# Kernel optimization log

Measured on AMD Instinct MI355X. Metric: run time of the kernel, lower is better.

## Reference

```python
import jax, jax.numpy as jnp
import numpy as np

# 8 voxel corner offsets in {0,1}^3 (order matches signed offsets in the
# torch module after the *0.5+0.5 remap used inside splitting/trilinear calls)
_CORNERS = np.array([[1,1,1],[1,1,0],[1,0,1],[0,1,1],[1,0,0],[0,1,0],[0,0,1],[0,0,0]], dtype=np.float32)

K = 150000   # unique corner keys (embedding rows)
V = 100000   # voxels
N = 262144   # query samples (rays * steps)
D = 64       # quantized_embed_dim


def setup_inputs() -> dict:
    key = jax.random.key(0)
    k1, k2, k3, k4, k5 = jax.random.split(key, 5)
    values = jax.random.normal(k1, (K, D), dtype=jnp.float32)
    p = jax.random.uniform(k2, (N, 3), dtype=jnp.float32)            # local trilinear coords in [0,1]
    W_proj = jax.random.normal(k3, (D, D), dtype=jnp.float32) / np.sqrt(D)
    b_proj = jnp.zeros((D,), dtype=jnp.float32)
    feats = jax.random.randint(k4, (V, 8), 0, K, dtype=jnp.int64) if jax.config.read('jax_enable_x64') else jax.random.randint(k4, (V, 8), 0, K).astype(jnp.int32)
    sample_vidx = jax.random.randint(k5, (N,), 0, V).astype(jnp.int32)
    return {"values": values, "p": p, "W_proj": W_proj, "b_proj": b_proj,
            "feats": feats, "sample_vidx": sample_vidx}


def trilinear_interp(p, q, corner_feats):
    # p: [N,3] in [0,1]; q: [8,3] corners in {0,1}; corner_feats: [N,8,D]
    # weight per corner = prod_d (p*q + (1-p)*(1-q))  -- identical to NSVF trilinear_interp
    w = jnp.prod(p[:, None, :] * q[None] + (1.0 - p[:, None, :]) * (1.0 - q[None]), axis=-1)  # [N,8]
    return jnp.einsum('nc,ncd->nd', w, corner_feats)


def reference(values, p, W_proj, b_proj, feats, sample_vidx):
    q = jnp.asarray(_CORNERS)
    corner_idx = feats[sample_vidx]          # [N,8] irregular gather of corner keys
    corner_feats = values[corner_idx]        # [N,8,D] embedding gather
    feat = trilinear_interp(p, q, corner_feats)   # [N,D]
    out = feat @ W_proj + b_proj             # values_proj Linear(embed_dim, embed_dim)
    return out
```

## Files before the change

### kernel.cpp

```cpp
#include <hip/hip_runtime.h>

#define TPB 256

typedef __attribute__((ext_vector_type(8))) short bf16x8;
typedef __attribute__((ext_vector_type(4))) float f32x4;

__device__ __forceinline__ unsigned pack_bf16_rne(float lo, float hi) {
    union { float f; unsigned u; } a, b;
    a.f = lo; b.f = hi;
    unsigned ua = (a.u + 0x7fffu + ((a.u >> 16) & 1u)) >> 16;
    unsigned ub = (b.u + 0x7fffu + ((b.u >> 16) & 1u)) >> 16;
    return ua | (ub << 16);
}
__device__ __forceinline__ float bf_lo(unsigned u) {
    union { unsigned i; float f; } c; c.i = u << 16; return c.f;
}
__device__ __forceinline__ float bf_hi(unsigned u) {
    union { unsigned i; float f; } c; c.i = u & 0xffff0000u; return c.f;
}

__global__ __launch_bounds__(TPB) void cvt_inputs(
    const float4* __restrict__ src, uint4* __restrict__ dst, int n8,
    const float* __restrict__ W, uint4* __restrict__ wfrag, int nvb)
{
    if ((int)blockIdx.x == nvb) {
        const int t = threadIdx.x;
        for (int e = t; e < 512; e += TPB) {
            const int l  = e & 63;
            const int f  = e >> 6;
            const int ct = f >> 1;
            const int kf = f & 1;
            const int col = ct * 16 + (l & 15);
            const int k0  = kf * 32 + 8 * (l >> 4);
            uint4 o;
            o.x = pack_bf16_rne(W[(k0 + 0) * 64 + col], W[(k0 + 1) * 64 + col]);
            o.y = pack_bf16_rne(W[(k0 + 2) * 64 + col], W[(k0 + 3) * 64 + col]);
            o.z = pack_bf16_rne(W[(k0 + 4) * 64 + col], W[(k0 + 5) * 64 + col]);
            o.w = pack_bf16_rne(W[(k0 + 6) * 64 + col], W[(k0 + 7) * 64 + col]);
            wfrag[e] = o;
        }
        return;
    }
    const int i = blockIdx.x * TPB + threadIdx.x;
    if (i < n8) {
        const float4 a = src[2 * i];
        const float4 b = src[2 * i + 1];
        uint4 o;
        o.x = pack_bf16_rne(a.x, a.y);
        o.y = pack_bf16_rne(a.z, a.w);
        o.z = pack_bf16_rne(b.x, b.y);
        o.w = pack_bf16_rne(b.z, b.w);
        dst[i] = o;
    }
}

__global__ __launch_bounds__(TPB, 2) void fused_embed_proj_mfma(
    const unsigned* __restrict__ valbf,
    const float* __restrict__ p,
    const uint4* __restrict__ wfrag,
    const float* __restrict__ b,
    const int*   __restrict__ feats,
    const int*   __restrict__ vidx,
    float* __restrict__ out,
    int N)
{
    const int t    = threadIdx.x;
    const int l    = t & 63;
    const int w    = t >> 6;
    const int base = blockIdx.x * 64 + 16 * w;
    const int srow = l & 15;
    const int kq   = l >> 4;

    int n = base + srow;
    if (n >= N) n = N - 1;

    const int v = vidx[n];
    const int4 f0 = *(const int4*)&feats[(size_t)v * 8];
    const int4 f1 = *(const int4*)&feats[(size_t)v * 8 + 4];

    const float px = p[n * 3 + 0];
    const float py = p[n * 3 + 1];
    const float pz = p[n * 3 + 2];
    const float ox = 1.0f - px, oy = 1.0f - py, oz = 1.0f - pz;
    float wgt[8];
    wgt[0] = px * py * pz;
    wgt[1] = px * py * oz;
    wgt[2] = px * oy * pz;
    wgt[3] = ox * py * pz;
    wgt[4] = px * oy * oz;
    wgt[5] = ox * py * oz;
    wgt[6] = ox * oy * pz;
    wgt[7] = ox * oy * oz;
    const int cidx[8] = {f0.x, f0.y, f0.z, f0.w, f1.x, f1.y, f1.z, f1.w};

    uint4 q0s[8], q1s[8];
    #pragma unroll
    for (int c = 0; c < 8; ++c) {
        const unsigned* row = valbf + (size_t)cidx[c] * 32;
        q0s[c] = *(const uint4*)(row + 4 * kq);
        q1s[c] = *(const uint4*)(row + 16 + 4 * kq);
    }

    float a0[8] = {0.f,0.f,0.f,0.f,0.f,0.f,0.f,0.f};
    float a1[8] = {0.f,0.f,0.f,0.f,0.f,0.f,0.f,0.f};
    #pragma unroll
    for (int c = 0; c < 8; ++c) {
        const uint4 q0 = q0s[c];
        const uint4 q1 = q1s[c];
        const float wc = wgt[c];
        a0[0] = fmaf(wc, bf_lo(q0.x), a0[0]);
        a0[1] = fmaf(wc, bf_hi(q0.x), a0[1]);
        a0[2] = fmaf(wc, bf_lo(q0.y), a0[2]);
        a0[3] = fmaf(wc, bf_hi(q0.y), a0[3]);
        a0[4] = fmaf(wc, bf_lo(q0.z), a0[4]);
        a0[5] = fmaf(wc, bf_hi(q0.z), a0[5]);
        a0[6] = fmaf(wc, bf_lo(q0.w), a0[6]);
        a0[7] = fmaf(wc, bf_hi(q0.w), a0[7]);
        a1[0] = fmaf(wc, bf_lo(q1.x), a1[0]);
        a1[1] = fmaf(wc, bf_hi(q1.x), a1[1]);
        a1[2] = fmaf(wc, bf_lo(q1.y), a1[2]);
        a1[3] = fmaf(wc, bf_hi(q1.y), a1[3]);
        a1[4] = fmaf(wc, bf_lo(q1.z), a1[4]);
        a1[5] = fmaf(wc, bf_hi(q1.z), a1[5]);
        a1[6] = fmaf(wc, bf_lo(q1.w), a1[6]);
        a1[7] = fmaf(wc, bf_hi(q1.w), a1[7]);
    }

    bf16x8 afrag0, afrag1;
    {
        union { unsigned u[4]; bf16x8 v; } cv;
        cv.u[0] = pack_bf16_rne(a0[0], a0[1]);
        cv.u[1] = pack_bf16_rne(a0[2], a0[3]);
        cv.u[2] = pack_bf16_rne(a0[4], a0[5]);
        cv.u[3] = pack_bf16_rne(a0[6], a0[7]);
        afrag0 = cv.v;
        cv.u[0] = pack_bf16_rne(a1[0], a1[1]);
        cv.u[1] = pack_bf16_rne(a1[2], a1[3]);
        cv.u[2] = pack_bf16_rne(a1[4], a1[5]);
        cv.u[3] = pack_bf16_rne(a1[6], a1[7]);
        afrag1 = cv.v;
    }

    #pragma unroll
    for (int ct = 0; ct < 4; ++ct) {
        const float bias = b[ct * 16 + srow];
        f32x4 acc;
        acc[0] = bias; acc[1] = bias; acc[2] = bias; acc[3] = bias;
        union { uint4 u; bf16x8 v; } b0, b1;
        b0.u = wfrag[(ct * 2 + 0) * 64 + l];
        b1.u = wfrag[(ct * 2 + 1) * 64 + l];
        acc = __builtin_amdgcn_mfma_f32_16x16x32_bf16(afrag0, b0.v, acc, 0, 0, 0);
        acc = __builtin_amdgcn_mfma_f32_16x16x32_bf16(afrag1, b1.v, acc, 0, 0, 0);

        const int col = ct * 16 + srow;
        #pragma unroll
        for (int r = 0; r < 4; ++r) {
            const int n2 = base + 4 * kq + r;
            if (n2 < N)
                __builtin_nontemporal_store(acc[r], &out[(size_t)n2 * 64 + col]);
        }
    }
}

__global__ __launch_bounds__(TPB) void fused_embed_proj_fp32(
    const float* __restrict__ values, const float* __restrict__ p,
    const float* __restrict__ W, const float* __restrict__ b,
    const int* __restrict__ feats, const int* __restrict__ vidx,
    float* __restrict__ out, int N)
{
    __shared__ float featS[64][68];
    __shared__ float Wlds[64][64];

    const int t    = threadIdx.x;
    const int base = blockIdx.x * 64;
    {
        const float4* Wv = (const float4*)W;
        float4*       Wl = (float4*)&Wlds[0][0];
        #pragma unroll
        for (int i = 0; i < 4; ++i) Wl[t + i * TPB] = Wv[t + i * TPB];
    }
    const int g  = t & 15;
    const int sb = t >> 4;

    int   cidx[4][8];
    float wgt[4][8];
    #pragma unroll
    for (int i = 0; i < 4; ++i) {
        const int s = sb + 16 * i;
        int n = base + s;
        if (n >= N) n = N - 1;
        const int v = vidx[n];
        const int4 f0 = *(const int4*)&feats[(size_t)v * 8];
        const int4 f1 = *(const int4*)&feats[(size_t)v * 8 + 4];
        cidx[i][0] = f0.x; cidx[i][1] = f0.y; cidx[i][2] = f0.z; cidx[i][3] = f0.w;
        cidx[i][4] = f1.x; cidx[i][5] = f1.y; cidx[i][6] = f1.z; cidx[i][7] = f1.w;
        const float px = p[n * 3], py = p[n * 3 + 1], pz = p[n * 3 + 2];
        const float ox = 1.f - px, oy = 1.f - py, oz = 1.f - pz;
        wgt[i][0] = px * py * pz; wgt[i][1] = px * py * oz;
        wgt[i][2] = px * oy * pz; wgt[i][3] = ox * py * pz;
        wgt[i][4] = px * oy * oz; wgt[i][5] = ox * py * oz;
        wgt[i][6] = ox * oy * pz; wgt[i][7] = ox * oy * oz;
    }
    #pragma unroll
    for (int i = 0; i < 4; ++i) {
        float4 acc; acc.x = acc.y = acc.z = acc.w = 0.f;
        #pragma unroll
        for (int c = 0; c < 8; ++c) {
            const float4 val = *(const float4*)&values[(size_t)cidx[i][c] * 64 + 4 * g];
            const float w = wgt[i][c];
            acc.x = fmaf(w, val.x, acc.x); acc.y = fmaf(w, val.y, acc.y);
            acc.z = fmaf(w, val.z, acc.z); acc.w = fmaf(w, val.w, acc.w);
        }
        *(float4*)&featS[sb + 16 * i][4 * g] = acc;
    }
    __syncthreads();

    const int tx = t & 15, ty = t >> 4;
    float acc[4][4];
    {
        const float4 bb = ((const float4*)b)[tx];
        #pragma unroll
        for (int j = 0; j < 4; ++j) {
            acc[j][0] = bb.x; acc[j][1] = bb.y; acc[j][2] = bb.z; acc[j][3] = bb.w;
        }
    }
    #pragma unroll 4
    for (int d = 0; d < 64; ++d) {
        const float a0 = featS[4 * ty + 0][d];
        const float a1 = featS[4 * ty + 1][d];
        const float a2 = featS[4 * ty + 2][d];
        const float a3 = featS[4 * ty + 3][d];
        const float4 wr = *(const float4*)&Wlds[d][4 * tx];
        acc[0][0] = fmaf(a0, wr.x, acc[0][0]); acc[0][1] = fmaf(a0, wr.y, acc[0][1]);
        acc[0][2] = fmaf(a0, wr.z, acc[0][2]); acc[0][3] = fmaf(a0, wr.w, acc[0][3]);
        acc[1][0] = fmaf(a1, wr.x, acc[1][0]); acc[1][1] = fmaf(a1, wr.y, acc[1][1]);
        acc[1][2] = fmaf(a1, wr.z, acc[1][2]); acc[1][3] = fmaf(a1, wr.w, acc[1][3]);
        acc[2][0] = fmaf(a2, wr.x, acc[2][0]); acc[2][1] = fmaf(a2, wr.y, acc[2][1]);
        acc[2][2] = fmaf(a2, wr.z, acc[2][2]); acc[2][3] = fmaf(a2, wr.w, acc[2][3]);
        acc[3][0] = fmaf(a3, wr.x, acc[3][0]); acc[3][1] = fmaf(a3, wr.y, acc[3][1]);
        acc[3][2] = fmaf(a3, wr.z, acc[3][2]); acc[3][3] = fmaf(a3, wr.w, acc[3][3]);
    }
    #pragma unroll
    for (int j = 0; j < 4; ++j) {
        const int n = base + 4 * ty + j;
        if (n < N) {
            float4 o; o.x = acc[j][0]; o.y = acc[j][1]; o.z = acc[j][2]; o.w = acc[j][3];
            *(float4*)&out[(size_t)n * 64 + 4 * tx] = o;
        }
    }
}

extern "C" void kernel_launch(void* const* d_in, const int* in_sizes, int n_in,
                              void* d_out, int out_size, void* d_ws, size_t ws_size,
                              hipStream_t stream) {
    const float* values = (const float*)d_in[0];
    const float* p      = (const float*)d_in[1];
    const float* W      = (const float*)d_in[2];
    const float* b      = (const float*)d_in[3];
    const int*   feats  = (const int*)d_in[4];
    const int*   vidx   = (const int*)d_in[5];
    float* out = (float*)d_out;

    const int N  = in_sizes[5];
    const int KD = in_sizes[0];
    const int nblocks = (N + 63) / 64;

    const size_t val_bytes = (size_t)KD * 2;
    const size_t need      = val_bytes + 8192;
    if (ws_size >= need) {
        unsigned* valbf = (unsigned*)d_ws;
        uint4*    wfrag = (uint4*)((char*)d_ws + val_bytes);
        const int n8  = KD / 8;
        const int nvb = (n8 + TPB - 1) / TPB;
        cvt_inputs<<<nvb + 1, TPB, 0, stream>>>(
            (const float4*)values, (uint4*)valbf, n8, W, wfrag, nvb);
        fused_embed_proj_mfma<<<nblocks, TPB, 0, stream>>>(
            valbf, p, wfrag, b, feats, vidx, out, N);
    } else {
        fused_embed_proj_fp32<<<nblocks, TPB, 0, stream>>>(
            values, p, W, b, feats, vidx, out, N);
    }
}
```

Measured before the change: 68.62 us.

## Project embedding table before gathering, replacing per-sample MFMA with table projection

Result: slower. 75.82 us (+10.5%).

```diff
diff --git a/kernel.cpp b/kernel.cpp
--- a/kernel.cpp
+++ b/kernel.cpp
@@ -19,45 +19,65 @@
     union { unsigned i; float f; } c; c.i = u & 0xffff0000u; return c.f;
 }
 
-__global__ __launch_bounds__(TPB) void cvt_inputs(
-    const float4* __restrict__ src, uint4* __restrict__ dst, int n8,
-    const float* __restrict__ W, uint4* __restrict__ wfrag, int nvb)
+__global__ __launch_bounds__(TPB) void proj_table_mfma(
+    const float* __restrict__ values,
+    const float* __restrict__ W,
+    unsigned short* __restrict__ vp,
+    int K)
 {
-    if ((int)blockIdx.x == nvb) {
-        const int t = threadIdx.x;
-        for (int e = t; e < 512; e += TPB) {
-            const int l  = e & 63;
-            const int f  = e >> 6;
-            const int ct = f >> 1;
-            const int kf = f & 1;
-            const int col = ct * 16 + (l & 15);
-            const int k0  = kf * 32 + 8 * (l >> 4);
-            uint4 o;
-            o.x = pack_bf16_rne(W[(k0 + 0) * 64 + col], W[(k0 + 1) * 64 + col]);
-            o.y = pack_bf16_rne(W[(k0 + 2) * 64 + col], W[(k0 + 3) * 64 + col]);
-            o.z = pack_bf16_rne(W[(k0 + 4) * 64 + col], W[(k0 + 5) * 64 + col]);
-            o.w = pack_bf16_rne(W[(k0 + 6) * 64 + col], W[(k0 + 7) * 64 + col]);
-            wfrag[e] = o;
-        }
-        return;
-    }
-    const int i = blockIdx.x * TPB + threadIdx.x;
-    if (i < n8) {
-        const float4 a = src[2 * i];
-        const float4 b = src[2 * i + 1];
-        uint4 o;
-        o.x = pack_bf16_rne(a.x, a.y);
-        o.y = pack_bf16_rne(a.z, a.w);
-        o.z = pack_bf16_rne(b.x, b.y);
-        o.w = pack_bf16_rne(b.z, b.w);
-        dst[i] = o;
-    }
-}
-
-__global__ __launch_bounds__(TPB, 2) void fused_embed_proj_mfma(
-    const unsigned* __restrict__ valbf,
+    const int t    = threadIdx.x;
+    const int l    = t & 63;
+    const int w    = t >> 6;
+    const int r0   = blockIdx.x * 64 + 16 * w;
+    const int srow = l & 15;
+    const int kq   = l >> 4;
+
+    int row = r0 + srow;
+    if (row >= K) row = K - 1;
+
+    bf16x8 af[2];
+    #pragma unroll
+    for (int kf = 0; kf < 2; ++kf) {
+        const float4 x0 = *(const float4*)&values[(size_t)row * 64 + kf * 32 + 8 * kq];
+        const float4 x1 = *(const float4*)&values[(size_t)row * 64 + kf * 32 + 8 * kq + 4];
+        union { unsigned u[4]; bf16x8 v; } cv;
+        cv.u[0] = pack_bf16_rne(x0.x, x0.y);
+        cv.u[1] = pack_bf16_rne(x0.z, x0.w);
+        cv.u[2] = pack_bf16_rne(x1.x, x1.y);
+        cv.u[3] = pack_bf16_rne(x1.z, x1.w);
+        af[kf] = cv.v;
+    }
+
+    #pragma unroll
+    for (int ct = 0; ct < 4; ++ct) {
+        const int col = ct * 16 + srow;
+        f32x4 acc;
+        acc[0] = 0.f; acc[1] = 0.f; acc[2] = 0.f; acc[3] = 0.f;
+        #pragma unroll
+        for (int kf = 0; kf < 2; ++kf) {
+            const int k0 = kf * 32 + 8 * kq;
+            union { unsigned u[4]; bf16x8 v; } bv;
+            bv.u[0] = pack_bf16_rne(W[(k0 + 0) * 64 + col], W[(k0 + 1) * 64 + col]);
+            bv.u[1] = pack_bf16_rne(W[(k0 + 2) * 64 + col], W[(k0 + 3) * 64 + col]);
+            bv.u[2] = pack_bf16_rne(W[(k0 + 4) * 64 + col], W[(k0 + 5) * 64 + col]);
+            bv.u[3] = pack_bf16_rne(W[(k0 + 6) * 64 + col], W[(k0 + 7) * 64 + col]);
+            acc = __builtin_amdgcn_mfma_f32_16x16x32_bf16(af[kf], bv.v, acc, 0, 0, 0);
+        }
+        #pragma unroll
+        for (int r = 0; r < 4; ++r) {
+            const int orow = r0 + 4 * kq + r;
+            if (orow < K) {
+                union { float f; unsigned u; } a; a.f = acc[r];
+                const unsigned us = (a.u + 0x7fffu + ((a.u >> 16) & 1u)) >> 16;
+                vp[(size_t)orow * 64 + col] = (unsigned short)us;
+            }
+        }
+    }
+}
+
+__global__ __launch_bounds__(TPB) void gather_interp(
+    const unsigned* __restrict__ vp,
     const float* __restrict__ p,
-    const uint4* __restrict__ wfrag,
     const float* __restrict__ b,
     const int*   __restrict__ feats,
     const int*   __restrict__ vidx,
@@ -71,8 +91,9 @@
     const int srow = l & 15;
     const int kq   = l >> 4;
 
+    const bool valid = (base + srow) < N;
     int n = base + srow;
-    if (n >= N) n = N - 1;
+    if (!valid) n = N - 1;
 
     const int v = vidx[n];
     const int4 f0 = *(const int4*)&feats[(size_t)v * 8];
@@ -96,7 +117,7 @@
     uint4 q0s[8], q1s[8];
     #pragma unroll
     for (int c = 0; c < 8; ++c) {
-        const unsigned* row = valbf + (size_t)cidx[c] * 32;
+        const unsigned* row = vp + (size_t)cidx[c] * 32;
         q0s[c] = *(const uint4*)(row + 4 * kq);
         q1s[c] = *(const uint4*)(row + 16 + 4 * kq);
     }
@@ -126,39 +147,28 @@
         a1[7] = fmaf(wc, bf_hi(q1.w), a1[7]);
     }
 
-    bf16x8 afrag0, afrag1;
-    {
-        union { unsigned u[4]; bf16x8 v; } cv;
-        cv.u[0] = pack_bf16_rne(a0[0], a0[1]);
-        cv.u[1] = pack_bf16_rne(a0[2], a0[3]);
-        cv.u[2] = pack_bf16_rne(a0[4], a0[5]);
-        cv.u[3] = pack_bf16_rne(a0[6], a0[7]);
-        afrag0 = cv.v;
-        cv.u[0] = pack_bf16_rne(a1[0], a1[1]);
-        cv.u[1] = pack_bf16_rne(a1[2], a1[3]);
-        cv.u[2] = pack_bf16_rne(a1[4], a1[5]);
-        cv.u[3] = pack_bf16_rne(a1[6], a1[7]);
-        afrag1 = cv.v;
-    }
-
-    #pragma unroll
-    for (int ct = 0; ct < 4; ++ct) {
-        const float bias = b[ct * 16 + srow];
-        f32x4 acc;
-        acc[0] = bias; acc[1] = bias; acc[2] = bias; acc[3] = bias;
-        union { uint4 u; bf16x8 v; } b0, b1;
-        b0.u = wfrag[(ct * 2 + 0) * 64 + l];
-        b1.u = wfrag[(ct * 2 + 1) * 64 + l];
-        acc = __builtin_amdgcn_mfma_f32_16x16x32_bf16(afrag0, b0.v, acc, 0, 0, 0);
-        acc = __builtin_amdgcn_mfma_f32_16x16x32_bf16(afrag1, b1.v, acc, 0, 0, 0);
-
-        const int col = ct * 16 + srow;
-        #pragma unroll
-        for (int r = 0; r < 4; ++r) {
-            const int n2 = base + 4 * kq + r;
-            if (n2 < N)
-                __builtin_nontemporal_store(acc[r], &out[(size_t)n2 * 64 + col]);
-        }
+    if (valid) {
+        const float4 b00 = *(const float4*)&b[8 * kq];
+        const float4 b01 = *(const float4*)&b[8 * kq + 4];
+        const float4 b10 = *(const float4*)&b[32 + 8 * kq];
+        const float4 b11 = *(const float4*)&b[32 + 8 * kq + 4];
+        float* o = out + (size_t)n * 64;
+        __builtin_nontemporal_store(a0[0] + b00.x, o + 8 * kq + 0);
+        __builtin_nontemporal_store(a0[1] + b00.y, o + 8 * kq + 1);
+        __builtin_nontemporal_store(a0[2] + b00.z, o + 8 * kq + 2);
+        __builtin_nontemporal_store(a0[3] + b00.w, o + 8 * kq + 3);
+        __builtin_nontemporal_store(a0[4] + b01.x, o + 8 * kq + 4);
+        __builtin_nontemporal_store(a0[5] + b01.y, o + 8 * kq + 5);
+        __builtin_nontemporal_store(a0[6] + b01.z, o + 8 * kq + 6);
+        __builtin_nontemporal_store(a0[7] + b01.w, o + 8 * kq + 7);
+        __builtin_nontemporal_store(a1[0] + b10.x, o + 32 + 8 * kq + 0);
+        __builtin_nontemporal_store(a1[1] + b10.y, o + 32 + 8 * kq + 1);
+        __builtin_nontemporal_store(a1[2] + b10.z, o + 32 + 8 * kq + 2);
+        __builtin_nontemporal_store(a1[3] + b10.w, o + 32 + 8 * kq + 3);
+        __builtin_nontemporal_store(a1[4] + b11.x, o + 32 + 8 * kq + 4);
+        __builtin_nontemporal_store(a1[5] + b11.y, o + 32 + 8 * kq + 5);
+        __builtin_nontemporal_store(a1[6] + b11.z, o + 32 + 8 * kq + 6);
+        __builtin_nontemporal_store(a1[7] + b11.w, o + 32 + 8 * kq + 7);
     }
 }
 
@@ -263,19 +273,16 @@
 
     const int N  = in_sizes[5];
     const int KD = in_sizes[0];
+    const int K  = KD / 64;
     const int nblocks = (N + 63) / 64;
 
-    const size_t val_bytes = (size_t)KD * 2;
-    const size_t need      = val_bytes + 8192;
+    const size_t need = (size_t)KD * 2;
     if (ws_size >= need) {
-        unsigned* valbf = (unsigned*)d_ws;
-        uint4*    wfrag = (uint4*)((char*)d_ws + val_bytes);
-        const int n8  = KD / 8;
-        const int nvb = (n8 + TPB - 1) / TPB;
-        cvt_inputs<<<nvb + 1, TPB, 0, stream>>>(
-            (const float4*)values, (uint4*)valbf, n8, W, wfrag, nvb);
-        fused_embed_proj_mfma<<<nblocks, TPB, 0, stream>>>(
-            valbf, p, wfrag, b, feats, vidx, out, N);
+        unsigned short* vp = (unsigned short*)d_ws;
+        const int kblocks = (K + 63) / 64;
+        proj_table_mfma<<<kblocks, TPB, 0, stream>>>(values, W, vp, K);
+        gather_interp<<<nblocks, TPB, 0, stream>>>(
+            (const unsigned*)vp, p, b, feats, vidx, out, N);
     } else {
         fused_embed_proj_fp32<<<nblocks, TPB, 0, stream>>>(
             values, p, W, b, feats, vidx, out, N);
```

## Counting-sort samples by voxel before gather to improve corner-row locality

Applied to the files above, without the earlier changes.

Result: slower. 81.66 us (+19.0%).

```diff
diff --git a/kernel.cpp b/kernel.cpp
--- a/kernel.cpp
+++ b/kernel.cpp
@@ -19,48 +19,130 @@
     union { unsigned i; float f; } c; c.i = u & 0xffff0000u; return c.f;
 }
 
-__global__ __launch_bounds__(TPB) void cvt_inputs(
-    const float4* __restrict__ src, uint4* __restrict__ dst, int n8,
-    const float* __restrict__ W, uint4* __restrict__ wfrag, int nvb)
-{
-    if ((int)blockIdx.x == nvb) {
-        const int t = threadIdx.x;
-        for (int e = t; e < 512; e += TPB) {
-            const int l  = e & 63;
-            const int f  = e >> 6;
-            const int ct = f >> 1;
-            const int kf = f & 1;
-            const int col = ct * 16 + (l & 15);
-            const int k0  = kf * 32 + 8 * (l >> 4);
+__global__ __launch_bounds__(TPB) void prep_combo(
+    const float4* __restrict__ src, uint4* __restrict__ dst, int n8, int nvb,
+    unsigned* __restrict__ cnt, int V, int zb,
+    const float* __restrict__ W, uint4* __restrict__ wfrag)
+{
+    int bid = blockIdx.x;
+    if (bid < nvb) {
+        const int i = bid * TPB + threadIdx.x;
+        if (i < n8) {
+            const float4 a = src[2 * i];
+            const float4 b = src[2 * i + 1];
             uint4 o;
-            o.x = pack_bf16_rne(W[(k0 + 0) * 64 + col], W[(k0 + 1) * 64 + col]);
-            o.y = pack_bf16_rne(W[(k0 + 2) * 64 + col], W[(k0 + 3) * 64 + col]);
-            o.z = pack_bf16_rne(W[(k0 + 4) * 64 + col], W[(k0 + 5) * 64 + col]);
-            o.w = pack_bf16_rne(W[(k0 + 6) * 64 + col], W[(k0 + 7) * 64 + col]);
-            wfrag[e] = o;
+            o.x = pack_bf16_rne(a.x, a.y);
+            o.y = pack_bf16_rne(a.z, a.w);
+            o.z = pack_bf16_rne(b.x, b.y);
+            o.w = pack_bf16_rne(b.z, b.w);
+            dst[i] = o;
         }
         return;
     }
+    bid -= nvb;
+    if (bid < zb) {
+        const int i = bid * TPB + threadIdx.x;
+        if (i < V) cnt[i] = 0u;
+        return;
+    }
+    const int t = threadIdx.x;
+    for (int e = t; e < 512; e += TPB) {
+        const int l  = e & 63;
+        const int f  = e >> 6;
+        const int ct = f >> 1;
+        const int kf = f & 1;
+        const int col = ct * 16 + (l & 15);
+        const int k0  = kf * 32 + 8 * (l >> 4);
+        uint4 o;
+        o.x = pack_bf16_rne(W[(k0 + 0) * 64 + col], W[(k0 + 1) * 64 + col]);
+        o.y = pack_bf16_rne(W[(k0 + 2) * 64 + col], W[(k0 + 3) * 64 + col]);
+        o.z = pack_bf16_rne(W[(k0 + 4) * 64 + col], W[(k0 + 5) * 64 + col]);
+        o.w = pack_bf16_rne(W[(k0 + 6) * 64 + col], W[(k0 + 7) * 64 + col]);
+        wfrag[e] = o;
+    }
+}
+
+__global__ __launch_bounds__(TPB) void hist_kernel(
+    const int* __restrict__ vidx, unsigned* __restrict__ cnt, int N) {
     const int i = blockIdx.x * TPB + threadIdx.x;
-    if (i < n8) {
-        const float4 a = src[2 * i];
-        const float4 b = src[2 * i + 1];
-        uint4 o;
-        o.x = pack_bf16_rne(a.x, a.y);
-        o.y = pack_bf16_rne(a.z, a.w);
-        o.z = pack_bf16_rne(b.x, b.y);
-        o.w = pack_bf16_rne(b.z, b.w);
-        dst[i] = o;
-    }
-}
-
-__global__ __launch_bounds__(TPB, 2) void fused_embed_proj_mfma(
+    if (i < N) atomicAdd(&cnt[vidx[i]], 1u);
+}
+
+__global__ __launch_bounds__(TPB) void scan1_kernel(
+    const unsigned* __restrict__ cnt, unsigned* __restrict__ loc,
+    unsigned* __restrict__ chunksum, int V)
+{
+    __shared__ unsigned part[TPB];
+    const int t    = threadIdx.x;
+    const int base = blockIdx.x * 2048 + t * 8;
+
+    unsigned e[8];
+    unsigned s = 0;
+    #pragma unroll
+    for (int j = 0; j < 8; ++j) {
+        e[j] = (base + j < V) ? cnt[base + j] : 0u;
+        s += e[j];
+    }
+    part[t] = s;
+    __syncthreads();
+    for (int d = 1; d < TPB; d <<= 1) {
+        unsigned v = (t >= d) ? part[t - d] : 0u;
+        __syncthreads();
+        part[t] += v;
+        __syncthreads();
+    }
+    unsigned run = part[t] - s;
+    #pragma unroll
+    for (int j = 0; j < 8; ++j) {
+        if (base + j < V) loc[base + j] = run;
+        run += e[j];
+    }
+    if (t == TPB - 1) chunksum[blockIdx.x] = part[TPB - 1];
+}
+
+__global__ __launch_bounds__(TPB) void scan2_kernel(
+    const unsigned* __restrict__ chunksum, unsigned* __restrict__ chunkpref, int nc)
+{
+    __shared__ unsigned part[TPB];
+    const int t = threadIdx.x;
+    unsigned s = (t < nc) ? chunksum[t] : 0u;
+    part[t] = s;
+    __syncthreads();
+    for (int d = 1; d < TPB; d <<= 1) {
+        unsigned v = (t >= d) ? part[t - d] : 0u;
+        __syncthreads();
+        part[t] += v;
+        __syncthreads();
+    }
+    if (t < nc) chunkpref[t] = part[t] - s;
+}
+
+__global__ __launch_bounds__(TPB) void scatter_kernel(
+    const int* __restrict__ vidx, const float* __restrict__ p,
+    unsigned* __restrict__ loc, const unsigned* __restrict__ chunkpref,
+    float4* __restrict__ psort, int* __restrict__ svox, int N)
+{
+    const int i = blockIdx.x * TPB + threadIdx.x;
+    if (i < N) {
+        const int v = vidx[i];
+        const unsigned pos = chunkpref[v >> 11] + atomicAdd(&loc[v], 1u);
+        float4 r;
+        r.x = p[3 * i + 0];
+        r.y = p[3 * i + 1];
+        r.z = p[3 * i + 2];
+        r.w = __int_as_float(i);
+        psort[pos] = r;
+        svox[pos]  = v;
+    }
+}
+
+__global__ __launch_bounds__(TPB) void gather_mfma_sorted(
     const unsigned* __restrict__ valbf,
-    const float* __restrict__ p,
+    const float4* __restrict__ psort,
+    const int*   __restrict__ svox,
     const uint4* __restrict__ wfrag,
     const float* __restrict__ b,
     const int*   __restrict__ feats,
-    const int*   __restrict__ vidx,
     float* __restrict__ out,
     int N)
 {
@@ -71,16 +153,16 @@
     const int srow = l & 15;
     const int kq   = l >> 4;
 
-    int n = base + srow;
-    if (n >= N) n = N - 1;
-
-    const int v = vidx[n];
+    const int slot = base + srow;
+    const int cs   = (slot < N) ? slot : N - 1;
+
+    const float4 rec = psort[cs];
+    const int v = svox[cs];
+
     const int4 f0 = *(const int4*)&feats[(size_t)v * 8];
     const int4 f1 = *(const int4*)&feats[(size_t)v * 8 + 4];
 
-    const float px = p[n * 3 + 0];
-    const float py = p[n * 3 + 1];
-    const float pz = p[n * 3 + 2];
+    const float px = rec.x, py = rec.y, pz = rec.z;
     const float ox = 1.0f - px, oy = 1.0f - py, oz = 1.0f - pz;
     float wgt[8];
     wgt[0] = px * py * pz;
@@ -141,6 +223,116 @@
         afrag1 = cv.v;
     }
 
+    int nrow[4];
+    #pragma unroll
+    for (int r = 0; r < 4; ++r) {
+        const int s2 = base + 4 * kq + r;
+        nrow[r] = (s2 < N) ? __float_as_int(psort[s2].w) : -1;
+    }
+
+    #pragma unroll
+    for (int ct = 0; ct < 4; ++ct) {
+        const float bias = b[ct * 16 + srow];
+        f32x4 acc;
+        acc[0] = bias; acc[1] = bias; acc[2] = bias; acc[3] = bias;
+        union { uint4 u; bf16x8 v; } b0, b1;
+        b0.u = wfrag[(ct * 2 + 0) * 64 + l];
+        b1.u = wfrag[(ct * 2 + 1) * 64 + l];
+        acc = __builtin_amdgcn_mfma_f32_16x16x32_bf16(afrag0, b0.v, acc, 0, 0, 0);
+        acc = __builtin_amdgcn_mfma_f32_16x16x32_bf16(afrag1, b1.v, acc, 0, 0, 0);
+
+        const int col = ct * 16 + srow;
+        #pragma unroll
+        for (int r = 0; r < 4; ++r) {
+            if (nrow[r] >= 0)
+                __builtin_nontemporal_store(acc[r], &out[(size_t)nrow[r] * 64 + col]);
+        }
+    }
+}
+
+__global__ __launch_bounds__(TPB) void fused_embed_proj_mfma(
+    const unsigned* __restrict__ valbf, const float* __restrict__ p,
+    const uint4* __restrict__ wfrag, const float* __restrict__ b,
+    const int* __restrict__ feats, const int* __restrict__ vidx,
+    float* __restrict__ out, int N)
+{
+    const int t    = threadIdx.x;
+    const int l    = t & 63;
+    const int w    = t >> 6;
+    const int base = blockIdx.x * 64 + 16 * w;
+    const int srow = l & 15;
+    const int kq   = l >> 4;
+
+    int n = base + srow;
+    if (n >= N) n = N - 1;
+
+    const int v = vidx[n];
+    const int4 f0 = *(const int4*)&feats[(size_t)v * 8];
+    const int4 f1 = *(const int4*)&feats[(size_t)v * 8 + 4];
+
+    const float px = p[n * 3 + 0];
+    const float py = p[n * 3 + 1];
+    const float pz = p[n * 3 + 2];
+    const float ox = 1.0f - px, oy = 1.0f - py, oz = 1.0f - pz;
+    float wgt[8];
+    wgt[0] = px * py * pz;
+    wgt[1] = px * py * oz;
+    wgt[2] = px * oy * pz;
+    wgt[3] = ox * py * pz;
+    wgt[4] = px * oy * oz;
+    wgt[5] = ox * py * oz;
+    wgt[6] = ox * oy * pz;
+    wgt[7] = ox * oy * oz;
+    const int cidx[8] = {f0.x, f0.y, f0.z, f0.w, f1.x, f1.y, f1.z, f1.w};
+
+    uint4 q0s[8], q1s[8];
+    #pragma unroll
+    for (int c = 0; c < 8; ++c) {
+        const unsigned* row = valbf + (size_t)cidx[c] * 32;
+        q0s[c] = *(const uint4*)(row + 4 * kq);
+        q1s[c] = *(const uint4*)(row + 16 + 4 * kq);
+    }
+
+    float a0[8] = {0.f,0.f,0.f,0.f,0.f,0.f,0.f,0.f};
+    float a1[8] = {0.f,0.f,0.f,0.f,0.f,0.f,0.f,0.f};
+    #pragma unroll
+    for (int c = 0; c < 8; ++c) {
+        const uint4 q0 = q0s[c];
+        const uint4 q1 = q1s[c];
+        const float wc = wgt[c];
+        a0[0] = fmaf(wc, bf_lo(q0.x), a0[0]);
+        a0[1] = fmaf(wc, bf_hi(q0.x), a0[1]);
+        a0[2] = fmaf(wc, bf_lo(q0.y), a0[2]);
+        a0[3] = fmaf(wc, bf_hi(q0.y), a0[3]);
+        a0[4] = fmaf(wc, bf_lo(q0.z), a0[4]);
+        a0[5] = fmaf(wc, bf_hi(q0.z), a0[5]);
+        a0[6] = fmaf(wc, bf_lo(q0.w), a0[6]);
+        a0[7] = fmaf(wc, bf_hi(q0.w), a0[7]);
+        a1[0] = fmaf(wc, bf_lo(q1.x), a1[0]);
+        a1[1] = fmaf(wc, bf_hi(q1.x), a1[1]);
+        a1[2] = fmaf(wc, bf_lo(q1.y), a1[2]);
+        a1[3] = fmaf(wc, bf_hi(q1.y), a1[3]);
+        a1[4] = fmaf(wc, bf_lo(q1.z), a1[4]);
+        a1[5] = fmaf(wc, bf_hi(q1.z), a1[5]);
+        a1[6] = fmaf(wc, bf_lo(q1.w), a1[6]);
+        a1[7] = fmaf(wc, bf_hi(q1.w), a1[7]);
+    }
+
+    bf16x8 afrag0, afrag1;
+    {
+        union { unsigned u[4]; bf16x8 v; } cv;
+        cv.u[0] = pack_bf16_rne(a0[0], a0[1]);
+        cv.u[1] = pack_bf16_rne(a0[2], a0[3]);
+        cv.u[2] = pack_bf16_rne(a0[4], a0[5]);
+        cv.u[3] = pack_bf16_rne(a0[6], a0[7]);
+        afrag0 = cv.v;
+        cv.u[0] = pack_bf16_rne(a1[0], a1[1]);
+        cv.u[1] = pack_bf16_rne(a1[2], a1[3]);
+        cv.u[2] = pack_bf16_rne(a1[4], a1[5]);
+        cv.u[3] = pack_bf16_rne(a1[6], a1[7]);
+        afrag1 = cv.v;
+    }
+
     #pragma unroll
     for (int ct = 0; ct < 4; ++ct) {
         const float bias = b[ct * 16 + srow];
@@ -263,17 +455,49 @@
 
     const int N  = in_sizes[5];
     const int KD = in_sizes[0];
+    const int V  = in_sizes[4] / 8;
     const int nblocks = (N + 63) / 64;
-
-    const size_t val_bytes = (size_t)KD * 2;
-    const size_t need      = val_bytes + 8192;
-    if (ws_size >= need) {
-        unsigned* valbf = (unsigned*)d_ws;
-        uint4*    wfrag = (uint4*)((char*)d_ws + val_bytes);
-        const int n8  = KD / 8;
-        const int nvb = (n8 + TPB - 1) / TPB;
-        cvt_inputs<<<nvb + 1, TPB, 0, stream>>>(
-            (const float4*)values, (uint4*)valbf, n8, W, wfrag, nvb);
+    const int n8  = KD / 8;
+    const int nvb = (n8 + TPB - 1) / TPB;
+    const int zb  = (V + TPB - 1) / TPB;
+    const int nchunks = (V + 2047) / 2048;
+
+    auto align256 = [](size_t x) { return (x + 255) & ~(size_t)255; };
+    const size_t valbf_off = 0;
+    const size_t wfrag_off = align256((size_t)KD * 2);
+    const size_t cnt_off   = wfrag_off + align256((size_t)8192);
+    const size_t loc_off   = cnt_off + align256((size_t)V * 4);
+    const size_t csum_off  = loc_off + align256((size_t)V * 4);
+    const size_t cpref_off = csum_off + align256((size_t)nchunks * 4);
+    const size_t psort_off = cpref_off + align256((size_t)nchunks * 4);
+    const size_t svox_off  = psort_off + align256((size_t)N * 16);
+    const size_t need_sort = svox_off + align256((size_t)N * 4);
+    const size_t need_mfma = wfrag_off + 8192;
+
+    if (ws_size >= need_sort && nchunks <= TPB) {
+        unsigned* valbf  = (unsigned*)((char*)d_ws + valbf_off);
+        uint4*    wfrag  = (uint4*)((char*)d_ws + wfrag_off);
+        unsigned* cnt    = (unsigned*)((char*)d_ws + cnt_off);
+        unsigned* loc    = (unsigned*)((char*)d_ws + loc_off);
+        unsigned* csum   = (unsigned*)((char*)d_ws + csum_off);
+        unsigned* cpref  = (unsigned*)((char*)d_ws + cpref_off);
+        float4*   psort  = (float4*)((char*)d_ws + psort_off);
+        int*      svox   = (int*)((char*)d_ws + svox_off);
+
+        prep_combo<<<nvb + zb + 1, TPB, 0, stream>>>(
+            (const float4*)values, (uint4*)valbf, n8, nvb, cnt, V, zb, W, wfrag);
+        hist_kernel<<<(N + TPB - 1) / TPB, TPB, 0, stream>>>(vidx, cnt, N);
+        scan1_kernel<<<nchunks, TPB, 0, stream>>>(cnt, loc, csum, V);
+        scan2_kernel<<<1, TPB, 0, stream>>>(csum, cpref, nchunks);
+        scatter_kernel<<<(N + TPB - 1) / TPB, TPB, 0, stream>>>(
+            vidx, p, loc, cpref, psort, svox, N);
+        gather_mfma_sorted<<<nblocks, TPB, 0, stream>>>(
+            valbf, psort, svox, wfrag, b, feats, out, N);
+    } else if (ws_size >= need_mfma) {
+        unsigned* valbf = (unsigned*)((char*)d_ws + valbf_off);
+        uint4*    wfrag = (uint4*)((char*)d_ws + wfrag_off);
+        prep_combo<<<nvb + 1, TPB, 0, stream>>>(
+            (const float4*)values, (uint4*)valbf, n8, nvb, nullptr, 0, 0, W, wfrag);
         fused_embed_proj_mfma<<<nblocks, TPB, 0, stream>>>(
             valbf, p, wfrag, b, feats, vidx, out, N);
     } else {
```
